# Performance work log

Hardware: AMD Instinct MI355X
Metric: run time of the kernel (lower is better)

The kernel has to match this reference:

```python
import jax, jax.numpy as jnp
import numpy as np

EMB = 1024  # embedding_size in the torch module


def setup_inputs() -> dict:
    key = jax.random.key(0)
    ks = jax.random.split(key, 6)
    B, N, K = 64, 256, 4096
    y = jax.random.normal(ks[0], (B, N, 1024), dtype=jnp.float32)
    # nn.Linear weights, init normal(std=0.02), zero bias
    Wy_w = jax.random.normal(ks[1], (1024, 1024), dtype=jnp.float32) * 0.02  # [out,in]
    Wy_b = jnp.zeros((1024,), dtype=jnp.float32)
    Wz_w = jax.random.normal(ks[2], (1024, 2048), dtype=jnp.float32) * 0.02  # [out,in]
    Wz_b = jnp.zeros((1024,), dtype=jnp.float32)
    dic_z = jax.random.normal(ks[3], (K, 2048), dtype=jnp.float32)
    prior = jax.random.uniform(ks[4], (K,), dtype=jnp.float32)
    prior = prior / jnp.sum(prior)
    return {"y": y, "Wy_w": Wy_w, "Wy_b": Wy_b, "Wz_w": Wz_w, "Wz_b": Wz_b,
            "dic_z": dic_z, "prior": prior}


def reference(y, Wy_w, Wy_b, Wz_w, Wz_b, dic_z, prior):
    # h = Wy(y): [B,N,1024]; dz = Wz(dic_z): [K,1024]
    h = jnp.einsum('bni,oi->bno', y, Wy_w) + Wy_b
    dz = jnp.einsum('ki,oi->ko', dic_z, Wz_w) + Wz_b
    # attention over dictionary: [B,N,K]
    att = jax.nn.softmax(jnp.einsum('bnd,kd->bnk', h, dz) / jnp.sqrt(jnp.float32(EMB)), axis=-1)
    # z[b,n] = sum_k prior[k] * att[b,n,k] * dic_z[k]  -> [B,N,2048]
    # (avoids the [B,N,K,2048] intermediate the torch code materializes)
    z = jnp.einsum('bnk,k,ke->bne', att, prior, dic_z)
    return z
```

## Files before the change

kernel.cpp:

```cpp
#include <hip/hip_runtime.h>
#include <hip/hip_bf16.h>
#include <stdint.h>

typedef __bf16 bf16;
typedef __bf16 bf16x4 __attribute__((ext_vector_type(4)));
typedef __bf16 bf16x8 __attribute__((ext_vector_type(8)));
typedef float f32x4 __attribute__((ext_vector_type(4)));
typedef unsigned short ushort8 __attribute__((ext_vector_type(8)));

__device__ __forceinline__ void gload16(const bf16* g, char* l) {
  __builtin_amdgcn_global_load_lds(
      reinterpret_cast<const __attribute__((address_space(1))) unsigned int*>(
          reinterpret_cast<uintptr_t>(g)),
      reinterpret_cast<__attribute__((address_space(3))) unsigned int*>(
          reinterpret_cast<uintptr_t>(l)),
      16, 0, 0);
}

__global__ __launch_bounds__(256) void cast_bf16(const float* __restrict__ in,
                                                 bf16* __restrict__ out, int n8) {
  int i = blockIdx.x * blockDim.x + threadIdx.x;
  const int stride = gridDim.x * blockDim.x;
  for (; i < n8; i += stride) {
    const float4 v0 = reinterpret_cast<const float4*>(in)[i * 2];
    const float4 v1 = reinterpret_cast<const float4*>(in)[i * 2 + 1];
    bf16x8 o = { (bf16)v0.x, (bf16)v0.y, (bf16)v0.z, (bf16)v0.w,
                 (bf16)v1.x, (bf16)v1.y, (bf16)v1.z, (bf16)v1.w };
    reinterpret_cast<bf16x8*>(out)[i] = o;
  }
}

template <bool OUT_BF16, bool HAS_BIAS, int BN>
__global__ __launch_bounds__(512, 2) void gemm_pipe(
    const bf16* __restrict__ A, const bf16* __restrict__ B,
    const float* __restrict__ bias, void* __restrict__ Cout,
    int M, int N, int K, float scale) {
  constexpr int BM = 256;
  constexpr int SLOT = (BM + BN) * 64;
  constexpr int BOFF = BM * 64;
  constexpr int TM = (BN == 256) ? 128 : 64;
  constexpr int MI = TM / 16;
  constexpr int NI = 4;
  extern __shared__ char lds[];
  const int tid = threadIdx.x;
  const int lane = tid & 63, w = tid >> 6;

  const int gridN = N / BN;
  const int nwg = gridDim.x;
  const int orig = blockIdx.x;
  int wgid;
  { const int q = nwg >> 3, r = nwg & 7, x = orig & 7, rest = orig >> 3;
    wgid = (x < r ? x * (q + 1) : r * (q + 1) + (x - r) * q) + rest; }
  const int m0 = (wgid / gridN) * BM;
  const int n0 = (wgid % gridN) * BN;

  const int srow = w * 16 + (lane >> 2);
  const int scol = (((lane & 3) ^ ((srow >> 1) & 3))) * 8;
  const bf16* gA  = A + (size_t)(m0 + srow) * K + scol;
  const bf16* gA2 = gA + (size_t)128 * K;
  const bf16* gB  = B + (size_t)(n0 + srow) * K + scol;
  const bf16* gB2 = (BN == 256) ? gB + (size_t)128 * K : gB;

  auto stage = [&](int T) {
    char* sb = lds + (size_t)(T & 3) * SLOT;
    const int kc = T * 32;
    gload16(gA + kc,  sb + w * 1024);
    gload16(gA2 + kc, sb + 8192 + w * 1024);
    gload16(gB + kc,  sb + BOFF + w * 1024);
    if constexpr (BN == 256) gload16(gB2 + kc, sb + BOFF + 8192 + w * 1024);
  };

  const int fr = lane & 15, hi = lane >> 4;
  int wm, wn;
  if constexpr (BN == 256) { wm = w >> 2; wn = w & 3; }
  else                     { wm = w >> 1; wn = w & 1; }
  int aoff[MI], boff[NI];
#pragma unroll
  for (int mi = 0; mi < MI; ++mi) {
    const int row = wm * TM + mi * 16 + fr;
    aoff[mi] = row * 64 + ((hi ^ ((row >> 1) & 3)) << 4);
  }
#pragma unroll
  for (int ni = 0; ni < NI; ++ni) {
    const int row = wn * 64 + ni * 16 + fr;
    boff[ni] = BOFF + row * 64 + ((hi ^ ((row >> 1) & 3)) << 4);
  }

  f32x4 acc[MI][NI] = {};
  const int NT = K >> 5;

  stage(0); stage(1); stage(2);
  if constexpr (BN == 256) asm volatile("s_waitcnt vmcnt(8)" ::: "memory");
  else                     asm volatile("s_waitcnt vmcnt(6)" ::: "memory");
  __builtin_amdgcn_s_barrier();

  for (int t = 0; t < NT; ++t) {
    const char* sb = lds + (size_t)(t & 3) * SLOT;
    bf16x8 af[MI], bb[NI];
#pragma unroll
    for (int mi = 0; mi < MI; ++mi) af[mi] = *reinterpret_cast<const bf16x8*>(sb + aoff[mi]);
#pragma unroll
    for (int ni = 0; ni < NI; ++ni) bb[ni] = *reinterpret_cast<const bf16x8*>(sb + boff[ni]);
    if (t + 3 < NT) stage(t + 3);
    __builtin_amdgcn_s_barrier();
    __builtin_amdgcn_s_setprio(1);
#pragma unroll
    for (int mi = 0; mi < MI; ++mi)
#pragma unroll
      for (int ni = 0; ni < NI; ++ni)
        acc[mi][ni] = __builtin_amdgcn_mfma_f32_16x16x32_bf16(af[mi], bb[ni], acc[mi][ni], 0, 0, 0);
    __builtin_amdgcn_s_setprio(0);
    if (t + 3 < NT) {
      if constexpr (BN == 256) asm volatile("s_waitcnt vmcnt(8)" ::: "memory");
      else                     asm volatile("s_waitcnt vmcnt(6)" ::: "memory");
    } else if (t + 2 < NT) {
      if constexpr (BN == 256) asm volatile("s_waitcnt vmcnt(4)" ::: "memory");
      else                     asm volatile("s_waitcnt vmcnt(3)" ::: "memory");
    } else if (t + 1 < NT) {
      asm volatile("s_waitcnt vmcnt(0)" ::: "memory");
    }
    __builtin_amdgcn_s_barrier();
  }

  const int lro = hi * 4;
#pragma unroll
  for (int ni = 0; ni < NI; ++ni) {
    const int gcol = n0 + wn * 64 + ni * 16 + fr;
    float bvs = 0.f;
    if constexpr (HAS_BIAS) bvs = bias[gcol];
#pragma unroll
    for (int mi = 0; mi < MI; ++mi) {
      const int grow = m0 + wm * TM + mi * 16 + lro;
#pragma unroll
      for (int j = 0; j < 4; ++j) {
        const float c = acc[mi][ni][j] * scale + bvs;
        if constexpr (OUT_BF16)
          ((bf16*)Cout)[(size_t)(grow + j) * N + gcol] = (bf16)c;
        else
          ((float*)Cout)[(size_t)(grow + j) * N + gcol] = c;
      }
    }
  }
}

__global__ __launch_bounds__(256) void prep_w3t(const float* __restrict__ dic,
                                                const float* __restrict__ prior,
                                                bf16* __restrict__ w3t) {
  const int KD = 4096, E = 2048;
  __shared__ bf16 t[64][72];
  const int k0 = blockIdx.x * 64, e0 = blockIdx.y * 64;
  const int tid = threadIdx.x;
  const int er = (tid & 15) * 4;
  const int kr = tid >> 4;
#pragma unroll
  for (int p = 0; p < 4; ++p) {
    const int k = kr + p * 16;
    const float pr = prior[k0 + k];
    const float4 v = *reinterpret_cast<const float4*>(dic + (size_t)(k0 + k) * E + e0 + er);
    t[er + 0][k] = (bf16)(v.x * pr);
    t[er + 1][k] = (bf16)(v.y * pr);
    t[er + 2][k] = (bf16)(v.z * pr);
    t[er + 3][k] = (bf16)(v.w * pr);
  }
  __syncthreads();
  const int e = tid >> 2, kc = (tid & 3) * 16;
  ushort8 a = *reinterpret_cast<ushort8*>(&t[e][kc]);
  ushort8 b = *reinterpret_cast<ushort8*>(&t[e][kc + 8]);
  unsigned short* dst = (unsigned short*)w3t + (size_t)(e0 + e) * KD + k0 + kc;
  *reinterpret_cast<ushort8*>(dst) = a;
  *reinterpret_cast<ushort8*>(dst + 8) = b;
}

__global__ __launch_bounds__(256) void softmax_rows(unsigned short* __restrict__ S) {
  const int K = 4096;
  unsigned short* row = S + (size_t)blockIdx.x * K;
  const int tid = threadIdx.x;
  const int lane = tid & 63, w = tid >> 6;
  __shared__ float red[8];

  ushort8 v0 = *reinterpret_cast<const ushort8*>(row + tid * 8);
  ushort8 v1 = *reinterpret_cast<const ushort8*>(row + 2048 + tid * 8);
  float x[16];
#pragma unroll
  for (int i = 0; i < 8; ++i) {
    x[i]     = __uint_as_float(((unsigned)v0[i]) << 16);
    x[8 + i] = __uint_as_float(((unsigned)v1[i]) << 16);
  }
  float mx = x[0];
#pragma unroll
  for (int i = 1; i < 16; ++i) mx = fmaxf(mx, x[i]);
#pragma unroll
  for (int o = 32; o; o >>= 1) mx = fmaxf(mx, __shfl_xor(mx, o));
  if (lane == 0) red[w] = mx;
  __syncthreads();
  mx = fmaxf(fmaxf(red[0], red[1]), fmaxf(red[2], red[3]));

  float s = 0.f;
#pragma unroll
  for (int i = 0; i < 16; ++i) { x[i] = __expf(x[i] - mx); s += x[i]; }
#pragma unroll
  for (int o = 32; o; o >>= 1) s += __shfl_xor(s, o);
  if (lane == 0) red[4 + w] = s;
  __syncthreads();
  const float inv = 1.f / (red[4] + red[5] + red[6] + red[7]);

  ushort8 o0, o1;
#pragma unroll
  for (int i = 0; i < 8; ++i) {
    bf16 b0 = (bf16)(x[i] * inv);
    bf16 b1 = (bf16)(x[8 + i] * inv);
    o0[i] = __builtin_bit_cast(unsigned short, b0);
    o1[i] = __builtin_bit_cast(unsigned short, b1);
  }
  *reinterpret_cast<ushort8*>(row + tid * 8) = o0;
  *reinterpret_cast<ushort8*>(row + 2048 + tid * 8) = o1;
}

extern "C" void kernel_launch(void* const* d_in, const int* in_sizes, int n_in,
                              void* d_out, int out_size, void* d_ws, size_t ws_size,
                              hipStream_t stream) {
  const float* y     = (const float*)d_in[0];
  const float* Wy_w  = (const float*)d_in[1];
  const float* Wy_b  = (const float*)d_in[2];
  const float* Wz_w  = (const float*)d_in[3];
  const float* Wz_b  = (const float*)d_in[4];
  const float* dic   = (const float*)d_in[5];
  const float* prior = (const float*)d_in[6];
  float* z = (float*)d_out;

  const int M = 16384, D = 1024, E = 2048, KD = 4096;

  char* ws = (char*)d_ws;
  bf16* w3t  = (bf16*)(ws);
  bf16* h    = (bf16*)(ws + ((size_t)16 << 20));
  bf16* dzb  = (bf16*)(ws + ((size_t)48 << 20));
  bf16* S    = (bf16*)(ws + ((size_t)56 << 20));
  bf16* yb   = (bf16*)(ws + ((size_t)56 << 20));
  bf16* Wyb  = (bf16*)(ws + ((size_t)88 << 20));
  bf16* Wzb  = (bf16*)(ws + ((size_t)90 << 20));
  bf16* dicb = (bf16*)(ws + ((size_t)94 << 20));

  cast_bf16<<<2048, 256, 0, stream>>>(y, yb, M * D / 8);
  cast_bf16<<<512, 256, 0, stream>>>(Wy_w, Wyb, D * D / 8);
  cast_bf16<<<512, 256, 0, stream>>>(Wz_w, Wzb, D * E / 8);
  cast_bf16<<<1024, 256, 0, stream>>>(dic, dicb, KD * E / 8);
  prep_w3t<<<dim3(KD / 64, E / 64), 256, 0, stream>>>(dic, prior, w3t);
  gemm_pipe<true, true, 256><<<(M / 256) * (D / 256), 512, 131072, stream>>>(
      yb, Wyb, Wy_b, h, M, D, D, 1.0f);
  gemm_pipe<true, true, 128><<<(KD / 256) * (D / 128), 512, 98304, stream>>>(
      dicb, Wzb, Wz_b, dzb, KD, D, E, 1.0f);
  gemm_pipe<true, false, 256><<<(M / 256) * (KD / 256), 512, 131072, stream>>>(
      h, dzb, nullptr, S, M, KD, D, 0.03125f);
  softmax_rows<<<M, 256, 0, stream>>>((unsigned short*)S);
  gemm_pipe<false, false, 256><<<(M / 256) * (E / 256), 512, 131072, stream>>>(
      S, w3t, nullptr, z, M, E, KD, 1.0f);
}
```

Baseline: 577.0 us.

## Double-buffer LDS fragment registers to overlap next-tile reads with MFMA

Restructures the GEMM main loop so the LDS-to-register fragment loads for tile t+1 are issued while MFMAs for tile t execute. It uses ping-pong register sets, splits the A fragments into two halves interleaved with the MFMA halves, and unrolls the loop by two. The aim is to hide LDS read latency behind matrix work. In exchange it needs more VGPRs for the double-buffered fragments, which may pressure occupancy at launch_bounds(512,2), and it assumes NT is even.

```diff
diff --git a/kernel.cpp b/kernel.cpp
--- a/kernel.cpp
+++ b/kernel.cpp
@@ -16,6 +16,8 @@
           reinterpret_cast<uintptr_t>(l)),
       16, 0, 0);
 }
+
+#define VMCNT(n) asm volatile("s_waitcnt vmcnt(" #n ")" ::: "memory")
 
 __global__ __launch_bounds__(256) void cast_bf16(const float* __restrict__ in,
                                                  bf16* __restrict__ out, int n8) {
@@ -40,6 +42,7 @@
   constexpr int BOFF = BM * 64;
   constexpr int TM = (BN == 256) ? 128 : 64;
   constexpr int MI = TM / 16;
+  constexpr int MH = MI / 2;
   constexpr int NI = 4;
   extern __shared__ char lds[];
   const int tid = threadIdx.x;
@@ -74,53 +77,69 @@
   int wm, wn;
   if constexpr (BN == 256) { wm = w >> 2; wn = w & 3; }
   else                     { wm = w >> 1; wn = w & 1; }
-  int aoff[MI], boff[NI];
-#pragma unroll
-  for (int mi = 0; mi < MI; ++mi) {
-    const int row = wm * TM + mi * 16 + fr;
-    aoff[mi] = row * 64 + ((hi ^ ((row >> 1) & 3)) << 4);
-  }
-#pragma unroll
-  for (int ni = 0; ni < NI; ++ni) {
-    const int row = wn * 64 + ni * 16 + fr;
-    boff[ni] = BOFF + row * 64 + ((hi ^ ((row >> 1) & 3)) << 4);
-  }
+  const int arow = wm * TM + fr;
+  const int aoff0 = arow * 64 + ((hi ^ ((arow >> 1) & 3)) << 4);
+  const int brow = wn * 64 + fr;
+  const int boff0 = BOFF + brow * 64 + ((hi ^ ((brow >> 1) & 3)) << 4);
 
   f32x4 acc[MI][NI] = {};
   const int NT = K >> 5;
 
+  bf16x8 afA[MI], bbA[NI], afB[MI], bbB[NI];
+
   stage(0); stage(1); stage(2);
-  if constexpr (BN == 256) asm volatile("s_waitcnt vmcnt(8)" ::: "memory");
-  else                     asm volatile("s_waitcnt vmcnt(6)" ::: "memory");
+  if constexpr (BN == 256) VMCNT(8); else VMCNT(6);
   __builtin_amdgcn_s_barrier();
-
-  for (int t = 0; t < NT; ++t) {
-    const char* sb = lds + (size_t)(t & 3) * SLOT;
-    bf16x8 af[MI], bb[NI];
-#pragma unroll
-    for (int mi = 0; mi < MI; ++mi) af[mi] = *reinterpret_cast<const bf16x8*>(sb + aoff[mi]);
-#pragma unroll
-    for (int ni = 0; ni < NI; ++ni) bb[ni] = *reinterpret_cast<const bf16x8*>(sb + boff[ni]);
-    if (t + 3 < NT) stage(t + 3);
-    __builtin_amdgcn_s_barrier();
-    __builtin_amdgcn_s_setprio(1);
-#pragma unroll
-    for (int mi = 0; mi < MI; ++mi)
-#pragma unroll
-      for (int ni = 0; ni < NI; ++ni)
-        acc[mi][ni] = __builtin_amdgcn_mfma_f32_16x16x32_bf16(af[mi], bb[ni], acc[mi][ni], 0, 0, 0);
-    __builtin_amdgcn_s_setprio(0);
-    if (t + 3 < NT) {
-      if constexpr (BN == 256) asm volatile("s_waitcnt vmcnt(8)" ::: "memory");
-      else                     asm volatile("s_waitcnt vmcnt(6)" ::: "memory");
-    } else if (t + 2 < NT) {
-      if constexpr (BN == 256) asm volatile("s_waitcnt vmcnt(4)" ::: "memory");
-      else                     asm volatile("s_waitcnt vmcnt(3)" ::: "memory");
-    } else if (t + 1 < NT) {
-      asm volatile("s_waitcnt vmcnt(0)" ::: "memory");
-    }
-    __builtin_amdgcn_s_barrier();
-  }
+  {
+    const char* s0 = lds;
+#pragma unroll
+    for (int i = 0; i < NI; ++i) bbA[i] = *(const bf16x8*)(s0 + boff0 + i * 1024);
+#pragma unroll
+    for (int i = 0; i < MI; ++i) afA[i] = *(const bf16x8*)(s0 + aoff0 + i * 1024);
+  }
+
+#define GITER(T, AFc, BBc, AFn, BBn) do {                                      \
+    if ((T) + 3 < NT) {                                                        \
+      stage((T) + 3);                                                          \
+      if constexpr (BN == 256) VMCNT(8); else VMCNT(6);                        \
+    } else if ((T) + 2 < NT) {                                                 \
+      if constexpr (BN == 256) VMCNT(4); else VMCNT(3);                        \
+    } else if ((T) + 1 < NT) {                                                 \
+      VMCNT(0);                                                                \
+    }                                                                          \
+    __builtin_amdgcn_s_barrier();                                              \
+    const bool rd_ = (T) + 1 < NT;                                             \
+    const char* nb_ = lds + (size_t)(((T) + 1) & 3) * SLOT;                    \
+    if (rd_) {                                                                 \
+      _Pragma("unroll") for (int i = 0; i < NI; ++i)                           \
+        BBn[i] = *(const bf16x8*)(nb_ + boff0 + i * 1024);                     \
+      _Pragma("unroll") for (int i = 0; i < MH; ++i)                           \
+        AFn[i] = *(const bf16x8*)(nb_ + aoff0 + i * 1024);                     \
+    }                                                                          \
+    __builtin_amdgcn_s_setprio(1);                                             \
+    _Pragma("unroll") for (int mi = 0; mi < MH; ++mi)                          \
+      _Pragma("unroll") for (int ni = 0; ni < NI; ++ni)                        \
+        acc[mi][ni] = __builtin_amdgcn_mfma_f32_16x16x32_bf16(                 \
+            AFc[mi], BBc[ni], acc[mi][ni], 0, 0, 0);                           \
+    __builtin_amdgcn_s_setprio(0);                                             \
+    if (rd_) {                                                                 \
+      _Pragma("unroll") for (int i = MH; i < MI; ++i)                          \
+        AFn[i] = *(const bf16x8*)(nb_ + aoff0 + i * 1024);                     \
+    }                                                                          \
+    __builtin_amdgcn_s_setprio(1);                                             \
+    _Pragma("unroll") for (int mi = MH; mi < MI; ++mi)                         \
+      _Pragma("unroll") for (int ni = 0; ni < NI; ++ni)                        \
+        acc[mi][ni] = __builtin_amdgcn_mfma_f32_16x16x32_bf16(                 \
+            AFc[mi], BBc[ni], acc[mi][ni], 0, 0, 0);                           \
+    __builtin_amdgcn_s_setprio(0);                                             \
+    __builtin_amdgcn_s_barrier();                                              \
+  } while (0)
+
+  for (int t = 0; t < NT; t += 2) {
+    GITER(t, afA, bbA, afB, bbB);
+    GITER(t + 1, afB, bbB, afA, bbA);
+  }
+#undef GITER
 
   const int lro = hi * 4;
 #pragma unroll
```

New measurement: 582.2 us. About the same (+0.9%).

## Rewrite GEMM mainloop with K=64 double buffering and phased A/B staging

Applied to the files above, without the earlier changes.

Replaces the 4-slot K=32 ring-buffer GEMM with a double-buffered K=64 tile scheme. Loads for the next A tile and the tile after next for B are spread across several MFMA phases within each iteration, and a new 128-byte row XOR swizzle is used. The aim is fewer barriers and waits per unit of K, and global loads interleaved more finely with MFMA work. In exchange there are more barriers per iteration and tighter buffer-reuse ordering. The B tile is overwritten in place while A goes to the other buffer, which risks hazards if the waits are mis-set.

```diff
diff --git a/kernel.cpp b/kernel.cpp
--- a/kernel.cpp
+++ b/kernel.cpp
@@ -3,7 +3,6 @@
 #include <stdint.h>
 
 typedef __bf16 bf16;
-typedef __bf16 bf16x4 __attribute__((ext_vector_type(4)));
 typedef __bf16 bf16x8 __attribute__((ext_vector_type(8)));
 typedef float f32x4 __attribute__((ext_vector_type(4)));
 typedef unsigned short ushort8 __attribute__((ext_vector_type(8)));
@@ -16,6 +15,11 @@
           reinterpret_cast<uintptr_t>(l)),
       16, 0, 0);
 }
+
+#define VMCNT(n)  asm volatile("s_waitcnt vmcnt(" #n ")" ::: "memory")
+#define LGKM0()   do { asm volatile("s_waitcnt lgkmcnt(0)" ::: "memory"); \
+                       __builtin_amdgcn_sched_barrier(0); } while (0)
+#define BAR()     __builtin_amdgcn_s_barrier()
 
 __global__ __launch_bounds__(256) void cast_bf16(const float* __restrict__ in,
                                                  bf16* __restrict__ out, int n8) {
@@ -31,16 +35,16 @@
 }
 
 template <bool OUT_BF16, bool HAS_BIAS, int BN>
-__global__ __launch_bounds__(512, 2) void gemm_pipe(
+__global__ __launch_bounds__(512, 2) void gemm8(
     const bf16* __restrict__ A, const bf16* __restrict__ B,
     const float* __restrict__ bias, void* __restrict__ Cout,
     int M, int N, int K, float scale) {
-  constexpr int BM = 256;
-  constexpr int SLOT = (BM + BN) * 64;
-  constexpr int BOFF = BM * 64;
+  constexpr int BUFSZ = 32768 + BN * 128;
+  constexpr int BOFF = 32768;
   constexpr int TM = (BN == 256) ? 128 : 64;
   constexpr int MI = TM / 16;
   constexpr int NI = 4;
+  constexpr int NPH = MI / 2;
   extern __shared__ char lds[];
   const int tid = threadIdx.x;
   const int lane = tid & 63, w = tid >> 6;
@@ -51,76 +55,145 @@
   int wgid;
   { const int q = nwg >> 3, r = nwg & 7, x = orig & 7, rest = orig >> 3;
     wgid = (x < r ? x * (q + 1) : r * (q + 1) + (x - r) * q) + rest; }
-  const int m0 = (wgid / gridN) * BM;
+  const int m0 = (wgid / gridN) * 256;
   const int n0 = (wgid % gridN) * BN;
 
-  const int srow = w * 16 + (lane >> 2);
-  const int scol = (((lane & 3) ^ ((srow >> 1) & 3))) * 8;
-  const bf16* gA  = A + (size_t)(m0 + srow) * K + scol;
-  const bf16* gA2 = gA + (size_t)128 * K;
-  const bf16* gB  = B + (size_t)(n0 + srow) * K + scol;
-  const bf16* gB2 = (BN == 256) ? gB + (size_t)128 * K : gB;
-
-  auto stage = [&](int T) {
-    char* sb = lds + (size_t)(T & 3) * SLOT;
-    const int kc = T * 32;
-    gload16(gA + kc,  sb + w * 1024);
-    gload16(gA2 + kc, sb + 8192 + w * 1024);
-    gload16(gB + kc,  sb + BOFF + w * 1024);
-    if constexpr (BN == 256) gload16(gB2 + kc, sb + BOFF + 8192 + w * 1024);
+  const int srow = lane >> 3;
+  const int scol = ((lane & 7) ^ srow) * 8;
+  const bf16* gA = A + (size_t)(m0 + w * 8 + srow) * K + scol;
+  const bf16* gB = B + (size_t)(n0 + w * 8 + srow) * K + scol;
+
+  auto stA = [&](char* dst, int u, int h) {
+    gload16(gA + (size_t)(h * 128) * K + (size_t)u * 64, dst + h * 16384 + w * 1024);
+    gload16(gA + (size_t)(h * 128 + 64) * K + (size_t)u * 64, dst + h * 16384 + 8192 + w * 1024);
+  };
+  auto stB = [&](char* dst, int u, int h) {
+    gload16(gB + (size_t)(h * 128) * K + (size_t)u * 64, dst + BOFF + h * 16384 + w * 1024);
+    gload16(gB + (size_t)(h * 128 + 64) * K + (size_t)u * 64, dst + BOFF + h * 16384 + 8192 + w * 1024);
   };
 
   const int fr = lane & 15, hi = lane >> 4;
   int wm, wn;
   if constexpr (BN == 256) { wm = w >> 2; wn = w & 3; }
   else                     { wm = w >> 1; wn = w & 1; }
-  int aoff[MI], boff[NI];
-#pragma unroll
-  for (int mi = 0; mi < MI; ++mi) {
-    const int row = wm * TM + mi * 16 + fr;
-    aoff[mi] = row * 64 + ((hi ^ ((row >> 1) & 3)) << 4);
-  }
-#pragma unroll
-  for (int ni = 0; ni < NI; ++ni) {
-    const int row = wn * 64 + ni * 16 + fr;
-    boff[ni] = BOFF + row * 64 + ((hi ^ ((row >> 1) & 3)) << 4);
-  }
+  const int abase = (wm * TM + fr) * 128 + ((hi ^ (fr & 7)) << 4);
+  const int bbase = BOFF + (wn * 64 + fr) * 128 + ((hi ^ (fr & 7)) << 4);
+#define RD_A(b, mi, ks) (*(const bf16x8*)((b) + ((abase + (mi) * 2048) ^ ((ks) << 6))))
+#define RD_B(b, ni, ks) (*(const bf16x8*)((b) + ((bbase + (ni) * 2048) ^ ((ks) << 6))))
 
   f32x4 acc[MI][NI] = {};
-  const int NT = K >> 5;
-
-  stage(0); stage(1); stage(2);
-  if constexpr (BN == 256) asm volatile("s_waitcnt vmcnt(8)" ::: "memory");
-  else                     asm volatile("s_waitcnt vmcnt(6)" ::: "memory");
-  __builtin_amdgcn_s_barrier();
-
-  for (int t = 0; t < NT; ++t) {
-    const char* sb = lds + (size_t)(t & 3) * SLOT;
-    bf16x8 af[MI], bb[NI];
-#pragma unroll
-    for (int mi = 0; mi < MI; ++mi) af[mi] = *reinterpret_cast<const bf16x8*>(sb + aoff[mi]);
-#pragma unroll
-    for (int ni = 0; ni < NI; ++ni) bb[ni] = *reinterpret_cast<const bf16x8*>(sb + boff[ni]);
-    if (t + 3 < NT) stage(t + 3);
-    __builtin_amdgcn_s_barrier();
-    __builtin_amdgcn_s_setprio(1);
-#pragma unroll
-    for (int mi = 0; mi < MI; ++mi)
-#pragma unroll
-      for (int ni = 0; ni < NI; ++ni)
-        acc[mi][ni] = __builtin_amdgcn_mfma_f32_16x16x32_bf16(af[mi], bb[ni], acc[mi][ni], 0, 0, 0);
-    __builtin_amdgcn_s_setprio(0);
-    if (t + 3 < NT) {
-      if constexpr (BN == 256) asm volatile("s_waitcnt vmcnt(8)" ::: "memory");
-      else                     asm volatile("s_waitcnt vmcnt(6)" ::: "memory");
-    } else if (t + 2 < NT) {
-      if constexpr (BN == 256) asm volatile("s_waitcnt vmcnt(4)" ::: "memory");
-      else                     asm volatile("s_waitcnt vmcnt(3)" ::: "memory");
-    } else if (t + 1 < NT) {
-      asm volatile("s_waitcnt vmcnt(0)" ::: "memory");
+  const int NT = K >> 6;
+
+  stA(lds, 0, 0); stA(lds, 0, 1);
+  stB(lds, 0, 0);
+  if constexpr (BN == 256) stB(lds, 0, 1);
+  stB(lds + BUFSZ, 1, 0);
+  if constexpr (BN == 256) { stB(lds + BUFSZ, 1, 1); VMCNT(4); }
+  else                     { VMCNT(2); }
+  BAR();
+
+  for (int u = 0; u < NT; ++u) {
+    char* b  = lds + (size_t)(u & 1) * BUFSZ;
+    char* bn = lds + (size_t)((u + 1) & 1) * BUFSZ;
+    bf16x8 bb[2][NI], a[2][2];
+    const bool sA = (u + 1) < NT, sB = (u + 2) < NT;
+
+    if constexpr (BN == 256) {
+      a[0][0] = RD_A(b, 0, 0); a[0][1] = RD_A(b, 0, 1);
+      a[1][0] = RD_A(b, 1, 0); a[1][1] = RD_A(b, 1, 1);
+#pragma unroll
+      for (int ni = 0; ni < NI; ++ni) { bb[0][ni] = RD_B(b, ni, 0); bb[1][ni] = RD_B(b, ni, 1); }
+      if (sA) stA(bn, u + 1, 0);
+      BAR(); LGKM0();
+      __builtin_amdgcn_s_setprio(1);
+#pragma unroll
+      for (int m2 = 0; m2 < 2; ++m2)
+#pragma unroll
+        for (int ni = 0; ni < NI; ++ni) {
+          acc[m2][ni] = __builtin_amdgcn_mfma_f32_16x16x32_bf16(a[m2][0], bb[0][ni], acc[m2][ni], 0, 0, 0);
+          acc[m2][ni] = __builtin_amdgcn_mfma_f32_16x16x32_bf16(a[m2][1], bb[1][ni], acc[m2][ni], 0, 0, 0);
+        }
+      __builtin_amdgcn_s_setprio(0);
+      BAR();
+      a[0][0] = RD_A(b, 2, 0); a[0][1] = RD_A(b, 2, 1);
+      a[1][0] = RD_A(b, 3, 0); a[1][1] = RD_A(b, 3, 1);
+      if (sA) stA(bn, u + 1, 1);
+      BAR(); LGKM0();
+      __builtin_amdgcn_s_setprio(1);
+#pragma unroll
+      for (int m2 = 0; m2 < 2; ++m2)
+#pragma unroll
+        for (int ni = 0; ni < NI; ++ni) {
+          acc[2 + m2][ni] = __builtin_amdgcn_mfma_f32_16x16x32_bf16(a[m2][0], bb[0][ni], acc[2 + m2][ni], 0, 0, 0);
+          acc[2 + m2][ni] = __builtin_amdgcn_mfma_f32_16x16x32_bf16(a[m2][1], bb[1][ni], acc[2 + m2][ni], 0, 0, 0);
+        }
+      __builtin_amdgcn_s_setprio(0);
+      BAR();
+      a[0][0] = RD_A(b, 4, 0); a[0][1] = RD_A(b, 4, 1);
+      a[1][0] = RD_A(b, 5, 0); a[1][1] = RD_A(b, 5, 1);
+      if (sB) stB(b, u + 2, 0);
+      BAR(); LGKM0();
+      __builtin_amdgcn_s_setprio(1);
+#pragma unroll
+      for (int m2 = 0; m2 < 2; ++m2)
+#pragma unroll
+        for (int ni = 0; ni < NI; ++ni) {
+          acc[4 + m2][ni] = __builtin_amdgcn_mfma_f32_16x16x32_bf16(a[m2][0], bb[0][ni], acc[4 + m2][ni], 0, 0, 0);
+          acc[4 + m2][ni] = __builtin_amdgcn_mfma_f32_16x16x32_bf16(a[m2][1], bb[1][ni], acc[4 + m2][ni], 0, 0, 0);
+        }
+      __builtin_amdgcn_s_setprio(0);
+      BAR();
+      a[0][0] = RD_A(b, 6, 0); a[0][1] = RD_A(b, 6, 1);
+      a[1][0] = RD_A(b, 7, 0); a[1][1] = RD_A(b, 7, 1);
+      if (sB) stB(b, u + 2, 1);
+      BAR(); LGKM0();
+      __builtin_amdgcn_s_setprio(1);
+#pragma unroll
+      for (int m2 = 0; m2 < 2; ++m2)
+#pragma unroll
+        for (int ni = 0; ni < NI; ++ni) {
+          acc[6 + m2][ni] = __builtin_amdgcn_mfma_f32_16x16x32_bf16(a[m2][0], bb[0][ni], acc[6 + m2][ni], 0, 0, 0);
+          acc[6 + m2][ni] = __builtin_amdgcn_mfma_f32_16x16x32_bf16(a[m2][1], bb[1][ni], acc[6 + m2][ni], 0, 0, 0);
+        }
+      __builtin_amdgcn_s_setprio(0);
+      if (sB) VMCNT(4); else VMCNT(0);
+      BAR();
+    } else {
+      a[0][0] = RD_A(b, 0, 0); a[0][1] = RD_A(b, 0, 1);
+      a[1][0] = RD_A(b, 1, 0); a[1][1] = RD_A(b, 1, 1);
+#pragma unroll
+      for (int ni = 0; ni < NI; ++ni) { bb[0][ni] = RD_B(b, ni, 0); bb[1][ni] = RD_B(b, ni, 1); }
+      if (sA) { stA(bn, u + 1, 0); stA(bn, u + 1, 1); }
+      BAR(); LGKM0();
+      __builtin_amdgcn_s_setprio(1);
+#pragma unroll
+      for (int m2 = 0; m2 < 2; ++m2)
+#pragma unroll
+        for (int ni = 0; ni < NI; ++ni) {
+          acc[m2][ni] = __builtin_amdgcn_mfma_f32_16x16x32_bf16(a[m2][0], bb[0][ni], acc[m2][ni], 0, 0, 0);
+          acc[m2][ni] = __builtin_amdgcn_mfma_f32_16x16x32_bf16(a[m2][1], bb[1][ni], acc[m2][ni], 0, 0, 0);
+        }
+      __builtin_amdgcn_s_setprio(0);
+      BAR();
+      a[0][0] = RD_A(b, 2, 0); a[0][1] = RD_A(b, 2, 1);
+      a[1][0] = RD_A(b, 3, 0); a[1][1] = RD_A(b, 3, 1);
+      if (sB) stB(b, u + 2, 0);
+      BAR(); LGKM0();
+      __builtin_amdgcn_s_setprio(1);
+#pragma unroll
+      for (int m2 = 0; m2 < 2; ++m2)
+#pragma unroll
+        for (int ni = 0; ni < NI; ++ni) {
+          acc[2 + m2][ni] = __builtin_amdgcn_mfma_f32_16x16x32_bf16(a[m2][0], bb[0][ni], acc[2 + m2][ni], 0, 0, 0);
+          acc[2 + m2][ni] = __builtin_amdgcn_mfma_f32_16x16x32_bf16(a[m2][1], bb[1][ni], acc[2 + m2][ni], 0, 0, 0);
+        }
+      __builtin_amdgcn_s_setprio(0);
+      if (sB) VMCNT(2); else VMCNT(0);
+      BAR();
     }
-    __builtin_amdgcn_s_barrier();
-  }
+  }
+#undef RD_A
+#undef RD_B
 
   const int lro = hi * 4;
 #pragma unroll
@@ -245,13 +318,13 @@
   cast_bf16<<<512, 256, 0, stream>>>(Wz_w, Wzb, D * E / 8);
   cast_bf16<<<1024, 256, 0, stream>>>(dic, dicb, KD * E / 8);
   prep_w3t<<<dim3(KD / 64, E / 64), 256, 0, stream>>>(dic, prior, w3t);
-  gemm_pipe<true, true, 256><<<(M / 256) * (D / 256), 512, 131072, stream>>>(
+  gemm8<true, true, 256><<<(M / 256) * (D / 256), 512, 131072, stream>>>(
       yb, Wyb, Wy_b, h, M, D, D, 1.0f);
-  gemm_pipe<true, true, 128><<<(KD / 256) * (D / 128), 512, 98304, stream>>>(
+  gemm8<true, true, 128><<<(KD / 256) * (D / 128), 512, 98304, stream>>>(
       dicb, Wzb, Wz_b, dzb, KD, D, E, 1.0f);
-  gemm_pipe<true, false, 256><<<(M / 256) * (KD / 256), 512, 131072, stream>>>(
+  gemm8<true, false, 256><<<(M / 256) * (KD / 256), 512, 131072, stream>>>(
       h, dzb, nullptr, S, M, KD, D, 0.03125f);
   softmax_rows<<<M, 256, 0, stream>>>((unsigned short*)S);
-  gemm_pipe<false, false, 256><<<(M / 256) * (E / 256), 512, 131072, stream>>>(
+  gemm8<false, false, 256><<<(M / 256) * (E / 256), 512, 131072, stream>>>(
       S, w3t, nullptr, z, M, E, KD, 1.0f);
 }
```

New measurement: 562.2 us. 2.6% less time.
